# Performance work log

Hardware: AMD Instinct MI355X
Metric: run time of the kernel (lower is better)

## Reference

```python
import jax, jax.numpy as jnp
import numpy as np

N_NODES = 100000
N_EDGES = 1600000
G_DIM, H1_DIM, H2_DIM = 128, 64, 64
N_REL = 8          # 2 * n_speakers**2, n_speakers=2
N_BASES = 30


def setup_inputs() -> dict:
    key = jax.random.key(0)
    ks = jax.random.split(key, 12)
    sc = lambda *s: 1.0 / np.sqrt(s[0])
    return {
        "node_features": jax.random.normal(ks[0], (N_NODES, G_DIM), jnp.float32),
        "edge_index": jax.random.randint(ks[1], (2, N_EDGES), 0, N_NODES),
        "edge_norm": jax.random.uniform(ks[2], (N_EDGES,), jnp.float32),
        "edge_type": jax.random.randint(ks[3], (N_EDGES,), 0, N_REL),
        # RGCNConv params (basis decomposition)
        "basis": jax.random.normal(ks[4], (N_BASES, G_DIM, H1_DIM), jnp.float32) * sc(G_DIM),
        "comp": jax.random.normal(ks[5], (N_REL, N_BASES), jnp.float32) * sc(N_BASES),
        "root": jax.random.normal(ks[6], (G_DIM, H1_DIM), jnp.float32) * sc(G_DIM),
        "bias1": jnp.zeros((H1_DIM,), jnp.float32),
        # GraphConv params
        "w_rel": jax.random.normal(ks[7], (H1_DIM, H2_DIM), jnp.float32) * sc(H1_DIM),
        "b_rel": jnp.zeros((H2_DIM,), jnp.float32),
        "w_root": jax.random.normal(ks[8], (H1_DIM, H2_DIM), jnp.float32) * sc(H1_DIM),
    }


def reference(node_features, edge_index, edge_norm, edge_type,
              basis, comp, root, bias1, w_rel, b_rel, w_root):
    N = node_features.shape[0]
    src, dst = edge_index[0], edge_index[1]

    # ---- RGCNConv: per-relation mean aggregation, basis-decomposed weights ----
    W = jnp.einsum('rb,bio->rio', comp, basis)          # [R, g, h1]
    x_src = node_features[src]                           # [E, g] gather
    out1 = node_features @ root + bias1                  # root + bias
    for r in range(N_REL):                               # fixed small relation set
        m = (edge_type == r).astype(node_features.dtype)  # [E]
        s = jax.ops.segment_sum(x_src * m[:, None], dst, num_segments=N)  # [N, g]
        cnt = jax.ops.segment_sum(m, dst, num_segments=N)                 # [N]
        h = s / jnp.maximum(cnt, 1.0)[:, None]            # mean aggr (0 if no edges)
        out1 = out1 + h @ W[r]

    # ---- GraphConv: sum of x_j * edge_weight -> lin_rel, plus lin_root ----
    agg = jax.ops.segment_sum(out1[src] * edge_norm[:, None], dst, num_segments=N)
    out2 = agg @ w_rel + b_rel + out1 @ w_root
    return out2
```

## Files before the change

### kernel.cpp

```cpp
#include <hip/hip_runtime.h>
#include <hip/hip_bf16.h>

#define NN 100000
#define NE 1600000
#define GD 128
#define H1 64
#define H2 64
#define NREL 8
#define NBASES 30
#define NBTOT 576

#define NPB 256
#define NBUCK ((NN + NPB - 1) / NPB)
#define NWGA 128
#define ECHUNK ((NE + NWGA - 1) / NWGA)

typedef __attribute__((ext_vector_type(8))) short bf16x8;
typedef __attribute__((ext_vector_type(4))) float f32x4;

static __device__ __forceinline__ unsigned short f2bf(float x) {
    __hip_bfloat16 h = __float2bfloat16(x);
    return *reinterpret_cast<unsigned short*>(&h);
}
static __device__ __forceinline__ float bf2f(unsigned short u) {
    return __uint_as_float(((unsigned)u) << 16);
}
static __device__ __forceinline__ float bflo(unsigned u) {
    return __uint_as_float(u << 16);
}
static __device__ __forceinline__ float bfhi(unsigned u) {
    return __uint_as_float(u & 0xffff0000u);
}

__global__ void prep_kernel(const float* __restrict__ basis,
                            const float* __restrict__ comp,
                            const float* __restrict__ root,
                            const float* __restrict__ w_rel,
                            const float* __restrict__ w_root,
                            unsigned short* __restrict__ WcatT,
                            unsigned short* __restrict__ B2T)
{
    int idx = blockIdx.x * blockDim.x + threadIdx.x;
    const int totalW = NBTOT * GD;
    if (idx < totalW) {
        int c = idx / GD;
        int i = idx % GD;
        float v;
        if (c < NREL * H1) {
            int r = c >> 6, o = c & 63;
            float acc = 0.f;
            #pragma unroll 5
            for (int b = 0; b < NBASES; ++b)
                acc += comp[r * NBASES + b] * basis[(b * GD + i) * H1 + o];
            v = acc;
        } else {
            v = root[i * H1 + (c - NREL * H1)];
        }
        WcatT[idx] = f2bf(v);
    } else {
        int j = idx - totalW;
        if (j < H2 * GD) {
            int o = j / GD, i = j % GD;
            float v = (i < H1) ? w_rel[i * H2 + o] : w_root[(i - H1) * H2 + o];
            B2T[j] = f2bf(v);
        }
    }
}

__global__ __launch_bounds__(512)
void bucket_count(const int* __restrict__ ei, unsigned* __restrict__ bcnt)
{
    __shared__ unsigned l[NBUCK];
    int t = threadIdx.x;
    int c0 = blockIdx.x * ECHUNK;
    int c1 = c0 + ECHUNK; if (c1 > NE) c1 = NE;
    for (int i = t; i < NBUCK; i += 512) l[i] = 0;
    __syncthreads();
    for (int e = c0 + t; e < c1; e += 512)
        atomicAdd(&l[ei[NE + e] >> 8], 1u);
    __syncthreads();
    for (int i = t; i < NBUCK; i += 512)
        if (l[i]) atomicAdd(&bcnt[i], l[i]);
}

__global__ __launch_bounds__(512)
void bucket_scan(const unsigned* __restrict__ bcnt,
                 unsigned* __restrict__ boff,
                 unsigned* __restrict__ bcur,
                 unsigned* __restrict__ off)
{
    __shared__ unsigned s[512];
    int t = threadIdx.x;
    unsigned v = (t < NBUCK) ? bcnt[t] : 0u;
    s[t] = v;
    __syncthreads();
    for (int st = 1; st < 512; st <<= 1) {
        unsigned u = (t >= st) ? s[t - st] : 0u;
        __syncthreads();
        s[t] += u;
        __syncthreads();
    }
    if (t < NBUCK) { boff[t] = s[t] - v; bcur[t] = s[t] - v; }
    if (t == 511) { boff[NBUCK] = s[511]; off[NN] = s[511]; }
}

__global__ __launch_bounds__(512)
void partition_a(const int* __restrict__ ei, const int* __restrict__ et,
                 const float* __restrict__ enorm,
                 unsigned* __restrict__ bcur,
                 uint2* __restrict__ tmp)
{
    __shared__ unsigned lcnt[NBUCK], wbase[NBUCK], lcur[NBUCK];
    int t = threadIdx.x;
    int c0 = blockIdx.x * ECHUNK;
    int c1 = c0 + ECHUNK; if (c1 > NE) c1 = NE;
    for (int i = t; i < NBUCK; i += 512) { lcnt[i] = 0; lcur[i] = 0; }
    __syncthreads();
    for (int e = c0 + t; e < c1; e += 512) {
        int dst = ei[NE + e];
        atomicAdd(&lcnt[dst >> 8], 1u);
    }
    __syncthreads();
    for (int i = t; i < NBUCK; i += 512)
        wbase[i] = atomicAdd(&bcur[i], lcnt[i]);
    __syncthreads();
    for (int e = c0 + t; e < c1; e += 512) {
        int src = ei[e], dst = ei[NE + e], r = et[e];
        int b = dst >> 8;
        unsigned pos = wbase[b] + atomicAdd(&lcur[b], 1u);
        unsigned dl = (unsigned)(dst & (NPB - 1));
        tmp[pos] = make_uint2((dl << 24) | ((unsigned)src << 3) | (unsigned)r,
                              __float_as_uint(enorm[e]));
    }
}

__global__ __launch_bounds__(512)
void partition_b(const unsigned* __restrict__ boff,
                 const uint2* __restrict__ tmp,
                 uint2* __restrict__ csr,
                 unsigned* __restrict__ off,
                 unsigned* __restrict__ cnt)
{
    __shared__ unsigned lcnt[NPB * NREL];
    __shared__ unsigned sscan[256];
    __shared__ unsigned lcur[NPB];
    int b = blockIdx.x, t = threadIdx.x;
    int nlo = b * NPB;
    int nn = NN - nlo; if (nn > NPB) nn = NPB;
    for (int i = t; i < NPB * NREL; i += 512) lcnt[i] = 0;
    __syncthreads();
    unsigned bstart = boff[b], bend = boff[b + 1];
    for (unsigned j = bstart + t; j < bend; j += 512) {
        unsigned x = tmp[j].x;
        atomicAdd(&lcnt[((x >> 24) << 3) | (x & 7u)], 1u);
    }
    __syncthreads();
    unsigned tot = 0;
    if (t < 256) {
        if (t < nn) {
            #pragma unroll
            for (int r = 0; r < NREL; ++r) tot += lcnt[t * NREL + r];
        }
        sscan[t] = tot;
    }
    __syncthreads();
    for (int st = 1; st < 256; st <<= 1) {
        unsigned u = (t < 256 && t >= st) ? sscan[t - st] : 0u;
        __syncthreads();
        if (t < 256) sscan[t] += u;
        __syncthreads();
    }
    if (t < nn) {
        unsigned ex = bstart + sscan[t] - tot;
        off[nlo + t] = ex;
        lcur[t] = ex;
        *reinterpret_cast<uint4*>(&cnt[(size_t)(nlo + t) * NREL]) =
            *reinterpret_cast<uint4*>(&lcnt[t * NREL]);
        *reinterpret_cast<uint4*>(&cnt[(size_t)(nlo + t) * NREL + 4]) =
            *reinterpret_cast<uint4*>(&lcnt[t * NREL + 4]);
    }
    __syncthreads();
    for (unsigned j = bstart + t; j < bend; j += 512) {
        uint2 rec = tmp[j];
        unsigned dl = rec.x >> 24;
        unsigned p = atomicAdd(&lcur[dl], 1u);
        csr[p] = make_uint2(rec.x & 0x00FFFFFFu, rec.y);
    }
}

template<int MODE>
__global__ __launch_bounds__(256)
void mfma_gemm(const void* __restrict__ Avoid,
               const unsigned short* __restrict__ Bt,
               int M,
               const float* __restrict__ bias,
               unsigned short* __restrict__ y,
               unsigned short* __restrict__ root1b,
               float* __restrict__ out)
{
    constexpr int NT = (MODE == 0) ? 9 : 1;
    __shared__ unsigned short Alds[128 * 128];
    __shared__ unsigned short Blds[64 * 128];

    int tid = threadIdx.x;
    int m0 = blockIdx.x * 128;
    int w = tid >> 6, l = tid & 63;
    int lr = l & 15, lk = l >> 4;

    uint4 breg0, breg1, breg2, breg3;
    {
        int c0 = (0 * 256 + tid) >> 4, s0 = tid & 15;
        int c1 = (1 * 256 + tid) >> 4;
        int c2 = (2 * 256 + tid) >> 4;
        int c3 = (3 * 256 + tid) >> 4;
        breg0 = *reinterpret_cast<const uint4*>(&Bt[(size_t)c0 * GD + s0 * 8]);
        breg1 = *reinterpret_cast<const uint4*>(&Bt[(size_t)c1 * GD + s0 * 8]);
        breg2 = *reinterpret_cast<const uint4*>(&Bt[(size_t)c2 * GD + s0 * 8]);
        breg3 = *reinterpret_cast<const uint4*>(&Bt[(size_t)c3 * GD + s0 * 8]);
    }

    if (MODE == 0) {
        const float* A = (const float*)Avoid;
        #pragma unroll
        for (int p = 0; p < 16; ++p) {
            int f = p * 256 + tid;
            int r = f >> 5;
            int c4 = f & 31;
            float4 av = make_float4(0.f, 0.f, 0.f, 0.f);
            if (m0 + r < M)
                av = *reinterpret_cast<const float4*>(&A[(size_t)(m0 + r) * GD + c4 * 4]);
            ushort4 bv;
            bv.x = f2bf(av.x); bv.y = f2bf(av.y); bv.z = f2bf(av.z); bv.w = f2bf(av.w);
            int slot = (c4 >> 1) ^ (r & 7);
            int byte = r * 256 + (slot << 4) + ((c4 & 1) << 3);
            *reinterpret_cast<ushort4*>(reinterpret_cast<char*>(Alds) + byte) = bv;
        }
    } else {
        const unsigned short* A = (const unsigned short*)Avoid;
        #pragma unroll
        for (int p = 0; p < 8; ++p) {
            int f = p * 256 + tid;
            int r = f >> 4;
            int slot = f & 15;
            uint4 v = make_uint4(0u, 0u, 0u, 0u);
            if (m0 + r < M)
                v = *reinterpret_cast<const uint4*>(&A[(size_t)(m0 + r) * GD + slot * 8]);
            int byte = r * 256 + ((slot ^ (r & 7)) << 4);
            *reinterpret_cast<uint4*>(reinterpret_cast<char*>(Alds) + byte) = v;
        }
    }

    {
        int c = (0 * 256 + tid) >> 4, s = tid & 15;
        *reinterpret_cast<uint4*>(reinterpret_cast<char*>(Blds) + c * 256 + ((s ^ (c & 7)) << 4)) = breg0;
        c = (1 * 256 + tid) >> 4;
        *reinterpret_cast<uint4*>(reinterpret_cast<char*>(Blds) + c * 256 + ((s ^ (c & 7)) << 4)) = breg1;
        c = (2 * 256 + tid) >> 4;
        *reinterpret_cast<uint4*>(reinterpret_cast<char*>(Blds) + c * 256 + ((s ^ (c & 7)) << 4)) = breg2;
        c = (3 * 256 + tid) >> 4;
        *reinterpret_cast<uint4*>(reinterpret_cast<char*>(Blds) + c * 256 + ((s ^ (c & 7)) << 4)) = breg3;
    }
    asm volatile("s_waitcnt lgkmcnt(0)" ::: "memory");
    __builtin_amdgcn_sched_barrier(0);
    __builtin_amdgcn_s_barrier();
    __builtin_amdgcn_sched_barrier(0);

    #pragma unroll 1
    for (int nt = 0; nt < NT; ++nt) {
        if (nt + 1 < NT) {
            int c = (0 * 256 + tid) >> 4, s = tid & 15;
            breg0 = *reinterpret_cast<const uint4*>(&Bt[(size_t)((nt + 1) * 64 + c) * GD + s * 8]);
            c = (1 * 256 + tid) >> 4;
            breg1 = *reinterpret_cast<const uint4*>(&Bt[(size_t)((nt + 1) * 64 + c) * GD + s * 8]);
            c = (2 * 256 + tid) >> 4;
            breg2 = *reinterpret_cast<const uint4*>(&Bt[(size_t)((nt + 1) * 64 + c) * GD + s * 8]);
            c = (3 * 256 + tid) >> 4;
            breg3 = *reinterpret_cast<const uint4*>(&Bt[(size_t)((nt + 1) * 64 + c) * GD + s * 8]);
        }

        f32x4 acc[2][4];
        #pragma unroll
        for (int i = 0; i < 2; ++i)
            #pragma unroll
            for (int j = 0; j < 4; ++j)
                acc[i][j] = (f32x4){0.f, 0.f, 0.f, 0.f};

        #pragma unroll
        for (int ks = 0; ks < 4; ++ks) {
            int q = 4 * ks + lk;
            int sA = q ^ (lr & 7);
            bf16x8 a0 = *reinterpret_cast<const bf16x8*>(
                reinterpret_cast<char*>(Alds) + (w * 32 + 0 * 16 + lr) * 256 + (sA << 4));
            bf16x8 a1 = *reinterpret_cast<const bf16x8*>(
                reinterpret_cast<char*>(Alds) + (w * 32 + 1 * 16 + lr) * 256 + (sA << 4));
            #pragma unroll
            for (int cf = 0; cf < 4; ++cf) {
                bf16x8 b = *reinterpret_cast<const bf16x8*>(
                    reinterpret_cast<char*>(Blds) + (cf * 16 + lr) * 256 + (sA << 4));
                acc[0][cf] = __builtin_amdgcn_mfma_f32_16x16x32_bf16(b, a0, acc[0][cf], 0, 0, 0);
                acc[1][cf] = __builtin_amdgcn_mfma_f32_16x16x32_bf16(b, a1, acc[1][cf], 0, 0, 0);
            }
        }

        #pragma unroll
        for (int rf = 0; rf < 2; ++rf) {
            int row = m0 + w * 32 + rf * 16 + lr;
            if (row < M) {
                #pragma unroll
                for (int cf = 0; cf < 4; ++cf) {
                    int cb = cf * 16 + lk * 4;
                    f32x4 v = acc[rf][cf];
                    if (MODE == 0) {
                        if (nt < 8) {
                            ushort4 pv;
                            pv.x = f2bf(v[0]); pv.y = f2bf(v[1]);
                            pv.z = f2bf(v[2]); pv.w = f2bf(v[3]);
                            *reinterpret_cast<ushort4*>(&y[(size_t)row * 512 + nt * 64 + cb]) = pv;
                        } else {
                            float4 bb = *reinterpret_cast<const float4*>(&bias[cb]);
                            ushort4 pv;
                            pv.x = f2bf(v[0] + bb.x); pv.y = f2bf(v[1] + bb.y);
                            pv.z = f2bf(v[2] + bb.z); pv.w = f2bf(v[3] + bb.w);
                            *reinterpret_cast<ushort4*>(&root1b[(size_t)row * 64 + cb]) = pv;
                        }
                    } else {
                        float4 bb = *reinterpret_cast<const float4*>(&bias[cb]);
                        float4 ov;
                        ov.x = v[0] + bb.x; ov.y = v[1] + bb.y;
                        ov.z = v[2] + bb.z; ov.w = v[3] + bb.w;
                        *reinterpret_cast<float4*>(&out[(size_t)row * 64 + cb]) = ov;
                    }
                }
            }
        }

        if (nt + 1 < NT) {
            asm volatile("s_waitcnt lgkmcnt(0)" ::: "memory");
            __builtin_amdgcn_sched_barrier(0);
            __builtin_amdgcn_s_barrier();
            __builtin_amdgcn_sched_barrier(0);
            int c = (0 * 256 + tid) >> 4, s = tid & 15;
            *reinterpret_cast<uint4*>(reinterpret_cast<char*>(Blds) + c * 256 + ((s ^ (c & 7)) << 4)) = breg0;
            c = (1 * 256 + tid) >> 4;
            *reinterpret_cast<uint4*>(reinterpret_cast<char*>(Blds) + c * 256 + ((s ^ (c & 7)) << 4)) = breg1;
            c = (2 * 256 + tid) >> 4;
            *reinterpret_cast<uint4*>(reinterpret_cast<char*>(Blds) + c * 256 + ((s ^ (c & 7)) << 4)) = breg2;
            c = (3 * 256 + tid) >> 4;
            *reinterpret_cast<uint4*>(reinterpret_cast<char*>(Blds) + c * 256 + ((s ^ (c & 7)) << 4)) = breg3;
            asm volatile("s_waitcnt lgkmcnt(0)" ::: "memory");
            __builtin_amdgcn_sched_barrier(0);
            __builtin_amdgcn_s_barrier();
            __builtin_amdgcn_sched_barrier(0);
        }
    }
}

__global__ void rgcn_aggregate(const unsigned* __restrict__ off,
                               const uint2* __restrict__ csr,
                               const unsigned* __restrict__ cnt,
                               const unsigned short* __restrict__ y,
                               const unsigned short* __restrict__ root1b,
                               unsigned short* __restrict__ abuf)
{
    int gid = blockIdx.x * blockDim.x + threadIdx.x;
    int n = gid >> 6;
    int l = gid & 63;
    if (n >= NN) return;
    int g = l >> 4;
    int sl = l & 15;
    unsigned myc = (l < NREL) ? cnt[(size_t)n * NREL + l] : 1u;
    float myinv = 1.0f / (float)(myc > 0u ? myc : 1u);
    unsigned s = off[n], e = off[n + 1];
    float a0 = 0.f, a1 = 0.f, a2 = 0.f, a3 = 0.f;
    float b0 = 0.f, b1 = 0.f, b2 = 0.f, b3 = 0.f;
    unsigned i = s;
    for (; i + 8 <= e; i += 8) {
        uint2 rA = csr[i + g];
        uint2 rB = csr[i + 4 + g];
        uint2 vA = *reinterpret_cast<const uint2*>(&y[(size_t)rA.x * 64 + sl * 4]);
        uint2 vB = *reinterpret_cast<const uint2*>(&y[(size_t)rB.x * 64 + sl * 4]);
        float wA = __shfl(myinv, (int)(rA.x & 7));
        float wB = __shfl(myinv, (int)(rB.x & 7));
        a0 += wA * bflo(vA.x); a1 += wA * bfhi(vA.x);
        a2 += wA * bflo(vA.y); a3 += wA * bfhi(vA.y);
        b0 += wB * bflo(vB.x); b1 += wB * bfhi(vB.x);
        b2 += wB * bflo(vB.y); b3 += wB * bfhi(vB.y);
    }
    if (i + 4 <= e) {
        uint2 rA = csr[i + g];
        uint2 vA = *reinterpret_cast<const uint2*>(&y[(size_t)rA.x * 64 + sl * 4]);
        float wA = __shfl(myinv, (int)(rA.x & 7));
        a0 += wA * bflo(vA.x); a1 += wA * bfhi(vA.x);
        a2 += wA * bflo(vA.y); a3 += wA * bfhi(vA.y);
        i += 4;
    }
    if (i < e) {
        unsigned idx = i + (unsigned)g;
        bool valid = idx < e;
        uint2 r = csr[valid ? idx : i];
        uint2 v = *reinterpret_cast<const uint2*>(&y[(size_t)r.x * 64 + sl * 4]);
        float w = __shfl(myinv, (int)(r.x & 7));
        if (!valid) w = 0.f;
        b0 += w * bflo(v.x); b1 += w * bfhi(v.x);
        b2 += w * bflo(v.y); b3 += w * bfhi(v.y);
    }
    a0 += b0; a1 += b1; a2 += b2; a3 += b3;
    a0 += __shfl_xor(a0, 16); a0 += __shfl_xor(a0, 32);
    a1 += __shfl_xor(a1, 16); a1 += __shfl_xor(a1, 32);
    a2 += __shfl_xor(a2, 16); a2 += __shfl_xor(a2, 32);
    a3 += __shfl_xor(a3, 16); a3 += __shfl_xor(a3, 32);
    if (g == 0) {
        uint2 rb = *reinterpret_cast<const uint2*>(&root1b[(size_t)n * 64 + sl * 4]);
        ushort4 pv;
        pv.x = f2bf(bflo(rb.x) + a0);
        pv.y = f2bf(bfhi(rb.x) + a1);
        pv.z = f2bf(bflo(rb.y) + a2);
        pv.w = f2bf(bfhi(rb.y) + a3);
        *reinterpret_cast<ushort4*>(&abuf[(size_t)n * 128 + 64 + sl * 4]) = pv;
    }
}

__global__ void graph_aggregate(const unsigned* __restrict__ off,
                                const uint2* __restrict__ csr,
                                unsigned short* __restrict__ abuf)
{
    int gid = blockIdx.x * blockDim.x + threadIdx.x;
    int n = gid >> 6;
    int l = gid & 63;
    if (n >= NN) return;
    int g = l >> 4;
    int sl = l & 15;
    unsigned s = off[n], e = off[n + 1];
    float a0 = 0.f, a1 = 0.f, a2 = 0.f, a3 = 0.f;
    float b0 = 0.f, b1 = 0.f, b2 = 0.f, b3 = 0.f;
    unsigned i = s;
    for (; i + 8 <= e; i += 8) {
        uint2 rA = csr[i + g];
        uint2 rB = csr[i + 4 + g];
        uint2 vA = *reinterpret_cast<const uint2*>(&abuf[(size_t)(rA.x >> 3) * 128 + 64 + sl * 4]);
        uint2 vB = *reinterpret_cast<const uint2*>(&abuf[(size_t)(rB.x >> 3) * 128 + 64 + sl * 4]);
        float wA = __uint_as_float(rA.y);
        float wB = __uint_as_float(rB.y);
        a0 += wA * bflo(vA.x); a1 += wA * bfhi(vA.x);
        a2 += wA * bflo(vA.y); a3 += wA * bfhi(vA.y);
        b0 += wB * bflo(vB.x); b1 += wB * bfhi(vB.x);
        b2 += wB * bflo(vB.y); b3 += wB * bfhi(vB.y);
    }
    if (i + 4 <= e) {
        uint2 rA = csr[i + g];
        uint2 vA = *reinterpret_cast<const uint2*>(&abuf[(size_t)(rA.x >> 3) * 128 + 64 + sl * 4]);
        float wA = __uint_as_float(rA.y);
        a0 += wA * bflo(vA.x); a1 += wA * bfhi(vA.x);
        a2 += wA * bflo(vA.y); a3 += wA * bfhi(vA.y);
        i += 4;
    }
    if (i < e) {
        unsigned idx = i + (unsigned)g;
        bool valid = idx < e;
        uint2 r = csr[valid ? idx : i];
        uint2 v = *reinterpret_cast<const uint2*>(&abuf[(size_t)(r.x >> 3) * 128 + 64 + sl * 4]);
        float w = valid ? __uint_as_float(r.y) : 0.f;
        b0 += w * bflo(v.x); b1 += w * bfhi(v.x);
        b2 += w * bflo(v.y); b3 += w * bfhi(v.y);
    }
    a0 += b0; a1 += b1; a2 += b2; a3 += b3;
    a0 += __shfl_xor(a0, 16); a0 += __shfl_xor(a0, 32);
    a1 += __shfl_xor(a1, 16); a1 += __shfl_xor(a1, 32);
    a2 += __shfl_xor(a2, 16); a2 += __shfl_xor(a2, 32);
    a3 += __shfl_xor(a3, 16); a3 += __shfl_xor(a3, 32);
    if (g == 0) {
        ushort4 pv;
        pv.x = f2bf(a0); pv.y = f2bf(a1); pv.z = f2bf(a2); pv.w = f2bf(a3);
        *reinterpret_cast<ushort4*>(&abuf[(size_t)n * 128 + sl * 4]) = pv;
    }
}

extern "C" void kernel_launch(void* const* d_in, const int* in_sizes, int n_in,
                              void* d_out, int out_size, void* d_ws, size_t ws_size,
                              hipStream_t stream)
{
    const float* node_features = (const float*)d_in[0];
    const int*   edge_index    = (const int*)d_in[1];
    const float* edge_norm     = (const float*)d_in[2];
    const int*   edge_type     = (const int*)d_in[3];
    const float* basis         = (const float*)d_in[4];
    const float* comp          = (const float*)d_in[5];
    const float* root          = (const float*)d_in[6];
    const float* bias1         = (const float*)d_in[7];
    const float* w_rel         = (const float*)d_in[8];
    const float* b_rel         = (const float*)d_in[9];
    const float* w_root        = (const float*)d_in[10];
    float* out = (float*)d_out;

    char* ws = (char*)d_ws;
    size_t o = 0;
    auto alloc = [&](size_t bytes) -> void* {
        o = (o + 511) & ~(size_t)511;
        void* p = ws + o;
        o += bytes;
        return p;
    };
    unsigned short* WcatT = (unsigned short*)alloc((size_t)NBTOT * GD * 2);
    unsigned short* B2T   = (unsigned short*)alloc((size_t)H2 * GD * 2);
    unsigned* cnt      = (unsigned*)alloc((size_t)NN * NREL * 4);
    unsigned* off_     = (unsigned*)alloc((size_t)(NN + 1) * 4);
    unsigned* bcnt     = (unsigned*)alloc((size_t)NBUCK * 4);
    unsigned* boff     = (unsigned*)alloc((size_t)(NBUCK + 1) * 4);
    unsigned* bcur     = (unsigned*)alloc((size_t)NBUCK * 4);
    uint2*    csr      = (uint2*)alloc((size_t)NE * 8);
    unsigned short* y  = (unsigned short*)alloc((size_t)NN * 512 * 2);
    unsigned short* root1b = (unsigned short*)alloc((size_t)NN * 64 * 2);
    unsigned short* abuf = (unsigned short*)alloc((size_t)NN * 128 * 2);
    uint2*    tmp      = (uint2*)abuf;

    hipMemsetAsync(bcnt, 0, (size_t)NBUCK * 4, stream);

    prep_kernel<<<(NBTOT * GD + H2 * GD + 255) / 256, 256, 0, stream>>>(
        basis, comp, root, w_rel, w_root, WcatT, B2T);

    bucket_count<<<NWGA, 512, 0, stream>>>(edge_index, bcnt);
    bucket_scan<<<1, 512, 0, stream>>>(bcnt, boff, bcur, off_);
    partition_a<<<NWGA, 512, 0, stream>>>(edge_index, edge_type, edge_norm, bcur, tmp);
    partition_b<<<NBUCK, 512, 0, stream>>>(boff, tmp, csr, off_, cnt);

    int gblk = (NN + 127) / 128;
    mfma_gemm<0><<<gblk, 256, 0, stream>>>(node_features, WcatT, NN, bias1, y, root1b, nullptr);

    rgcn_aggregate<<<(NN * 64 + 255) / 256, 256, 0, stream>>>(off_, csr, cnt, y, root1b, abuf);

    graph_aggregate<<<(NN * 64 + 255) / 256, 256, 0, stream>>>(off_, csr, abuf);

    mfma_gemm<1><<<gblk, 256, 0, stream>>>(abuf, B2T, NN, b_rel, nullptr, nullptr, out);
}
```

Before: 248.5 us.

## Co-schedule edge partitioning with the node GEMM in fused multi-role kernels

Weight prep and bucket counting now run in one kernel, split by block index. The first GEMM (node features times concatenated relation and root weights) is split in half: one half runs alongside partition_a and the other alongside partition_b, using shared-memory carve-outs and block-index dispatch. The GEMM body is reworked for 512-thread blocks with 16 rows per wave, and the second GEMM becomes its own specialised kernel. The aim is to fill idle compute units during the atomic-heavy partition phases and to cut launch count, at the cost of a larger shared-memory footprint per block and possibly different occupancy for the partition work.

```diff
diff --git a/kernel.cpp b/kernel.cpp
--- a/kernel.cpp
+++ b/kernel.cpp
@@ -14,6 +14,9 @@
 #define NBUCK ((NN + NPB - 1) / NPB)
 #define NWGA 128
 #define ECHUNK ((NE + NWGA - 1) / NWGA)
+#define PREP_BLKS 160
+#define GBLK ((NN + 127) / 128)
+#define GHALF 391
 
 typedef __attribute__((ext_vector_type(8))) short bf16x8;
 typedef __attribute__((ext_vector_type(4))) float f32x4;
@@ -32,55 +35,57 @@
     return __uint_as_float(u & 0xffff0000u);
 }
 
-__global__ void prep_kernel(const float* __restrict__ basis,
-                            const float* __restrict__ comp,
-                            const float* __restrict__ root,
-                            const float* __restrict__ w_rel,
-                            const float* __restrict__ w_root,
-                            unsigned short* __restrict__ WcatT,
-                            unsigned short* __restrict__ B2T)
-{
-    int idx = blockIdx.x * blockDim.x + threadIdx.x;
-    const int totalW = NBTOT * GD;
-    if (idx < totalW) {
-        int c = idx / GD;
-        int i = idx % GD;
-        float v;
-        if (c < NREL * H1) {
-            int r = c >> 6, o = c & 63;
-            float acc = 0.f;
-            #pragma unroll 5
-            for (int b = 0; b < NBASES; ++b)
-                acc += comp[r * NBASES + b] * basis[(b * GD + i) * H1 + o];
-            v = acc;
-        } else {
-            v = root[i * H1 + (c - NREL * H1)];
-        }
-        WcatT[idx] = f2bf(v);
-    } else {
-        int j = idx - totalW;
-        if (j < H2 * GD) {
-            int o = j / GD, i = j % GD;
-            float v = (i < H1) ? w_rel[i * H2 + o] : w_root[(i - H1) * H2 + o];
-            B2T[j] = f2bf(v);
-        }
-    }
-}
-
 __global__ __launch_bounds__(512)
-void bucket_count(const int* __restrict__ ei, unsigned* __restrict__ bcnt)
+void fused_pre(const float* __restrict__ basis,
+               const float* __restrict__ comp,
+               const float* __restrict__ root,
+               const float* __restrict__ w_rel,
+               const float* __restrict__ w_root,
+               unsigned short* __restrict__ WcatT,
+               unsigned short* __restrict__ B2T,
+               const int* __restrict__ ei,
+               unsigned* __restrict__ bcnt)
 {
     __shared__ unsigned l[NBUCK];
     int t = threadIdx.x;
-    int c0 = blockIdx.x * ECHUNK;
-    int c1 = c0 + ECHUNK; if (c1 > NE) c1 = NE;
-    for (int i = t; i < NBUCK; i += 512) l[i] = 0;
-    __syncthreads();
-    for (int e = c0 + t; e < c1; e += 512)
-        atomicAdd(&l[ei[NE + e] >> 8], 1u);
-    __syncthreads();
-    for (int i = t; i < NBUCK; i += 512)
-        if (l[i]) atomicAdd(&bcnt[i], l[i]);
+    if (blockIdx.x < PREP_BLKS) {
+        int idx = blockIdx.x * 512 + t;
+        const int totalW = NBTOT * GD;
+        if (idx < totalW) {
+            int c = idx / GD;
+            int i = idx % GD;
+            float v;
+            if (c < NREL * H1) {
+                int r = c >> 6, o = c & 63;
+                float acc = 0.f;
+                #pragma unroll 5
+                for (int b = 0; b < NBASES; ++b)
+                    acc += comp[r * NBASES + b] * basis[(b * GD + i) * H1 + o];
+                v = acc;
+            } else {
+                v = root[i * H1 + (c - NREL * H1)];
+            }
+            WcatT[idx] = f2bf(v);
+        } else {
+            int j = idx - totalW;
+            if (j < H2 * GD) {
+                int o = j / GD, i = j % GD;
+                float v = (i < H1) ? w_rel[i * H2 + o] : w_root[(i - H1) * H2 + o];
+                B2T[j] = f2bf(v);
+            }
+        }
+    } else {
+        int chunk = blockIdx.x - PREP_BLKS;
+        int c0 = chunk * ECHUNK;
+        int c1 = c0 + ECHUNK; if (c1 > NE) c1 = NE;
+        for (int i = t; i < NBUCK; i += 512) l[i] = 0;
+        __syncthreads();
+        for (int e = c0 + t; e < c1; e += 512)
+            atomicAdd(&l[ei[NE + e] >> 8], 1u);
+        __syncthreads();
+        for (int i = t; i < NBUCK; i += 512)
+            if (l[i]) atomicAdd(&bcnt[i], l[i]);
+    }
 }
 
 __global__ __launch_bounds__(512)
@@ -104,15 +109,133 @@
     if (t == 511) { boff[NBUCK] = s[511]; off[NN] = s[511]; }
 }
 
-__global__ __launch_bounds__(512)
-void partition_a(const int* __restrict__ ei, const int* __restrict__ et,
-                 const float* __restrict__ enorm,
-                 unsigned* __restrict__ bcur,
-                 uint2* __restrict__ tmp)
-{
-    __shared__ unsigned lcnt[NBUCK], wbase[NBUCK], lcur[NBUCK];
+__device__ __forceinline__
+void gemm0_body(char* smem, int m0,
+                const float* __restrict__ A,
+                const unsigned short* __restrict__ Bt,
+                int M,
+                const float* __restrict__ bias,
+                unsigned short* __restrict__ y,
+                unsigned short* __restrict__ root1b)
+{
+    unsigned short* Alds = (unsigned short*)smem;
+    unsigned short* Blds = (unsigned short*)(smem + 32768);
+    int tid = threadIdx.x;
+    int w = tid >> 6, l = tid & 63;
+    int lr = l & 15, lk = l >> 4;
+
+    uint4 breg0, breg1;
+    {
+        int c0 = tid >> 4, s0 = tid & 15;
+        int c1 = 32 + (tid >> 4);
+        breg0 = *reinterpret_cast<const uint4*>(&Bt[(size_t)c0 * GD + s0 * 8]);
+        breg1 = *reinterpret_cast<const uint4*>(&Bt[(size_t)c1 * GD + s0 * 8]);
+    }
+
+    #pragma unroll
+    for (int p = 0; p < 8; ++p) {
+        int f = p * 512 + tid;
+        int r = f >> 5;
+        int c4 = f & 31;
+        float4 av = make_float4(0.f, 0.f, 0.f, 0.f);
+        if (m0 + r < M)
+            av = *reinterpret_cast<const float4*>(&A[(size_t)(m0 + r) * GD + c4 * 4]);
+        ushort4 bv;
+        bv.x = f2bf(av.x); bv.y = f2bf(av.y); bv.z = f2bf(av.z); bv.w = f2bf(av.w);
+        int slot = (c4 >> 1) ^ (r & 7);
+        int byte = r * 256 + (slot << 4) + ((c4 & 1) << 3);
+        *reinterpret_cast<ushort4*>(reinterpret_cast<char*>(Alds) + byte) = bv;
+    }
+
+    {
+        int c = tid >> 4, s = tid & 15;
+        *reinterpret_cast<uint4*>(reinterpret_cast<char*>(Blds) + c * 256 + ((s ^ (c & 7)) << 4)) = breg0;
+        c = 32 + (tid >> 4);
+        *reinterpret_cast<uint4*>(reinterpret_cast<char*>(Blds) + c * 256 + ((s ^ (c & 7)) << 4)) = breg1;
+    }
+    asm volatile("s_waitcnt lgkmcnt(0)" ::: "memory");
+    __builtin_amdgcn_sched_barrier(0);
+    __builtin_amdgcn_s_barrier();
+    __builtin_amdgcn_sched_barrier(0);
+
+    #pragma unroll 1
+    for (int nt = 0; nt < 9; ++nt) {
+        if (nt + 1 < 9) {
+            int c = tid >> 4, s = tid & 15;
+            breg0 = *reinterpret_cast<const uint4*>(&Bt[(size_t)((nt + 1) * 64 + c) * GD + s * 8]);
+            c = 32 + (tid >> 4);
+            breg1 = *reinterpret_cast<const uint4*>(&Bt[(size_t)((nt + 1) * 64 + c) * GD + s * 8]);
+        }
+
+        f32x4 acc[4];
+        #pragma unroll
+        for (int j = 0; j < 4; ++j)
+            acc[j] = (f32x4){0.f, 0.f, 0.f, 0.f};
+
+        #pragma unroll
+        for (int ks = 0; ks < 4; ++ks) {
+            int q = 4 * ks + lk;
+            int sA = q ^ (lr & 7);
+            bf16x8 a0 = *reinterpret_cast<const bf16x8*>(
+                reinterpret_cast<char*>(Alds) + (w * 16 + lr) * 256 + (sA << 4));
+            #pragma unroll
+            for (int cf = 0; cf < 4; ++cf) {
+                bf16x8 b = *reinterpret_cast<const bf16x8*>(
+                    reinterpret_cast<char*>(Blds) + (cf * 16 + lr) * 256 + (sA << 4));
+                acc[cf] = __builtin_amdgcn_mfma_f32_16x16x32_bf16(b, a0, acc[cf], 0, 0, 0);
+            }
+        }
+
+        int row = m0 + w * 16 + lr;
+        if (row < M) {
+            #pragma unroll
+            for (int cf = 0; cf < 4; ++cf) {
+                int cb = cf * 16 + lk * 4;
+                f32x4 v = acc[cf];
+                if (nt < 8) {
+                    ushort4 pv;
+                    pv.x = f2bf(v[0]); pv.y = f2bf(v[1]);
+                    pv.z = f2bf(v[2]); pv.w = f2bf(v[3]);
+                    *reinterpret_cast<ushort4*>(&y[(size_t)row * 512 + nt * 64 + cb]) = pv;
+                } else {
+                    float4 bb = *reinterpret_cast<const float4*>(&bias[cb]);
+                    ushort4 pv;
+                    pv.x = f2bf(v[0] + bb.x); pv.y = f2bf(v[1] + bb.y);
+                    pv.z = f2bf(v[2] + bb.z); pv.w = f2bf(v[3] + bb.w);
+                    *reinterpret_cast<ushort4*>(&root1b[(size_t)row * 64 + cb]) = pv;
+                }
+            }
+        }
+
+        if (nt + 1 < 9) {
+            asm volatile("s_waitcnt lgkmcnt(0)" ::: "memory");
+            __builtin_amdgcn_sched_barrier(0);
+            __builtin_amdgcn_s_barrier();
+            __builtin_amdgcn_sched_barrier(0);
+            int c = tid >> 4, s = tid & 15;
+            *reinterpret_cast<uint4*>(reinterpret_cast<char*>(Blds) + c * 256 + ((s ^ (c & 7)) << 4)) = breg0;
+            c = 32 + (tid >> 4);
+            *reinterpret_cast<uint4*>(reinterpret_cast<char*>(Blds) + c * 256 + ((s ^ (c & 7)) << 4)) = breg1;
+            asm volatile("s_waitcnt lgkmcnt(0)" ::: "memory");
+            __builtin_amdgcn_sched_barrier(0);
+            __builtin_amdgcn_s_barrier();
+            __builtin_amdgcn_sched_barrier(0);
+        }
+    }
+}
+
+__device__ __forceinline__
+void parta_body(char* smem, int chunk,
+                const int* __restrict__ ei, const int* __restrict__ et,
+                const float* __restrict__ enorm,
+                unsigned* __restrict__ bcur,
+                uint2* __restrict__ tmp)
+{
+    unsigned* lcnt  = (unsigned*)smem;
+    unsigned* wbase = (unsigned*)(smem + 1600);
+    unsigned* lcur  = (unsigned*)(smem + 3200);
     int t = threadIdx.x;
-    int c0 = blockIdx.x * ECHUNK;
+    int c0 = chunk * ECHUNK;
     int c1 = c0 + ECHUNK; if (c1 > NE) c1 = NE;
     for (int i = t; i < NBUCK; i += 512) { lcnt[i] = 0; lcur[i] = 0; }
     __syncthreads();
@@ -134,17 +257,18 @@
     }
 }
 
-__global__ __launch_bounds__(512)
-void partition_b(const unsigned* __restrict__ boff,
-                 const uint2* __restrict__ tmp,
-                 uint2* __restrict__ csr,
-                 unsigned* __restrict__ off,
-                 unsigned* __restrict__ cnt)
-{
-    __shared__ unsigned lcnt[NPB * NREL];
-    __shared__ unsigned sscan[256];
-    __shared__ unsigned lcur[NPB];
-    int b = blockIdx.x, t = threadIdx.x;
+__device__ __forceinline__
+void partb_body(char* smem, int b,
+                const unsigned* __restrict__ boff,
+                const uint2* __restrict__ tmp,
+                uint2* __restrict__ csr,
+                unsigned* __restrict__ off,
+                unsigned* __restrict__ cnt)
+{
+    unsigned* lcnt  = (unsigned*)smem;
+    unsigned* sscan = (unsigned*)(smem + 8192);
+    unsigned* lcur  = (unsigned*)(smem + 9216);
+    int t = threadIdx.x;
     int nlo = b * NPB;
     int nn = NN - nlo; if (nn > NPB) nn = NPB;
     for (int i = t; i < NPB * NREL; i += 512) lcnt[i] = 0;
@@ -188,17 +312,50 @@
     }
 }
 
-template<int MODE>
+__global__ __launch_bounds__(512)
+void fused_a(const int* __restrict__ ei, const int* __restrict__ et,
+             const float* __restrict__ enorm,
+             unsigned* __restrict__ bcur,
+             uint2* __restrict__ tmp,
+             const float* __restrict__ A,
+             const unsigned short* __restrict__ Bt,
+             const float* __restrict__ bias,
+             unsigned short* __restrict__ y,
+             unsigned short* __restrict__ root1b)
+{
+    __shared__ char smem[49152];
+    if (blockIdx.x < NWGA)
+        parta_body(smem, blockIdx.x, ei, et, enorm, bcur, tmp);
+    else
+        gemm0_body(smem, (int)(blockIdx.x - NWGA) * 128, A, Bt, NN, bias, y, root1b);
+}
+
+__global__ __launch_bounds__(512)
+void fused_b(const unsigned* __restrict__ boff,
+             const uint2* __restrict__ tmp,
+             uint2* __restrict__ csr,
+             unsigned* __restrict__ off,
+             unsigned* __restrict__ cnt,
+             const float* __restrict__ A,
+             const unsigned short* __restrict__ Bt,
+             const float* __restrict__ bias,
+             unsigned short* __restrict__ y,
+             unsigned short* __restrict__ root1b)
+{
+    __shared__ char smem[49152];
+    if (blockIdx.x < NBUCK)
+        partb_body(smem, blockIdx.x, boff, tmp, csr, off, cnt);
+    else
+        gemm0_body(smem, (int)blockIdx.x * 128, A, Bt, NN, bias, y, root1b);
+}
+
 __global__ __launch_bounds__(256)
-void mfma_gemm(const void* __restrict__ Avoid,
-               const unsigned short* __restrict__ Bt,
-               int M,
-               const float* __restrict__ bias,
-               unsigned short* __restrict__ y,
-               unsigned short* __restrict__ root1b,
-               float* __restrict__ out)
-{
-    constexpr int NT = (MODE == 0) ? 9 : 1;
+void mfma_gemm1(const unsigned short* __restrict__ A,
+                const unsigned short* __restrict__ Bt,
+                int M,
+                const float* __restrict__ bias,
+                float* __restrict__ out)
+{
     __shared__ unsigned short Alds[128 * 128];
     __shared__ unsigned short Blds[64 * 128];
 
@@ -219,35 +376,16 @@
         breg3 = *reinterpret_cast<const uint4*>(&Bt[(size_t)c3 * GD + s0 * 8]);
     }
 
-    if (MODE == 0) {
-        const float* A = (const float*)Avoid;
-        #pragma unroll
-        for (int p = 0; p < 16; ++p) {
-            int f = p * 256 + tid;
-            int r = f >> 5;
-            int c4 = f & 31;
-            float4 av = make_float4(0.f, 0.f, 0.f, 0.f);
-            if (m0 + r < M)
-                av = *reinterpret_cast<const float4*>(&A[(size_t)(m0 + r) * GD + c4 * 4]);
-            ushort4 bv;
-            bv.x = f2bf(av.x); bv.y = f2bf(av.y); bv.z = f2bf(av.z); bv.w = f2bf(av.w);
-            int slot = (c4 >> 1) ^ (r & 7);
-            int byte = r * 256 + (slot << 4) + ((c4 & 1) << 3);
-            *reinterpret_cast<ushort4*>(reinterpret_cast<char*>(Alds) + byte) = bv;
-        }
-    } else {
-        const unsigned short* A = (const unsigned short*)Avoid;
-        #pragma unroll
-        for (int p = 0; p < 8; ++p) {
-            int f = p * 256 + tid;
-            int r = f >> 4;
-            int slot = f & 15;
-            uint4 v = make_uint4(0u, 0u, 0u, 0u);
-            if (m0 + r < M)
-                v = *reinterpret_cast<const uint4*>(&A[(size_t)(m0 + r) * GD + slot * 8]);
-            int byte = r * 256 + ((slot ^ (r & 7)) << 4);
-            *reinterpret_cast<uint4*>(reinterpret_cast<char*>(Alds) + byte) = v;
-        }
+    #pragma unroll
+    for (int p = 0; p < 8; ++p) {
+        int f = p * 256 + tid;
+        int r = f >> 4;
+        int slot = f & 15;
+        uint4 v = make_uint4(0u, 0u, 0u, 0u);
+        if (m0 + r < M)
+            v = *reinterpret_cast<const uint4*>(&A[(size_t)(m0 + r) * GD + slot * 8]);
+        int byte = r * 256 + ((slot ^ (r & 7)) << 4);
+        *reinterpret_cast<uint4*>(reinterpret_cast<char*>(Alds) + byte) = v;
     }
 
     {
@@ -260,97 +398,46 @@
         c = (3 * 256 + tid) >> 4;
         *reinterpret_cast<uint4*>(reinterpret_cast<char*>(Blds) + c * 256 + ((s ^ (c & 7)) << 4)) = breg3;
     }
-    asm volatile("s_waitcnt lgkmcnt(0)" ::: "memory");
-    __builtin_amdgcn_sched_barrier(0);
-    __builtin_amdgcn_s_barrier();
-    __builtin_amdgcn_sched_barrier(0);
-
-    #pragma unroll 1
-    for (int nt = 0; nt < NT; ++nt) {
-        if (nt + 1 < NT) {
-            int c = (0 * 256 + tid) >> 4, s = tid & 15;
-            breg0 = *reinterpret_cast<const uint4*>(&Bt[(size_t)((nt + 1) * 64 + c) * GD + s * 8]);
-            c = (1 * 256 + tid) >> 4;
-            breg1 = *reinterpret_cast<const uint4*>(&Bt[(size_t)((nt + 1) * 64 + c) * GD + s * 8]);
-            c = (2 * 256 + tid) >> 4;
-            breg2 = *reinterpret_cast<const uint4*>(&Bt[(size_t)((nt + 1) * 64 + c) * GD + s * 8]);
-            c = (3 * 256 + tid) >> 4;
-            breg3 = *reinterpret_cast<const uint4*>(&Bt[(size_t)((nt + 1) * 64 + c) * GD + s * 8]);
-        }
-
-        f32x4 acc[2][4];
+    __syncthreads();
+
+    f32x4 acc[2][4];
+    #pragma unroll
+    for (int i = 0; i < 2; ++i)
         #pragma unroll
-        for (int i = 0; i < 2; ++i)
-            #pragma unroll
-            for (int j = 0; j < 4; ++j)
-                acc[i][j] = (f32x4){0.f, 0.f, 0.f, 0.f};
-
+        for (int j = 0; j < 4; ++j)
+            acc[i][j] = (f32x4){0.f, 0.f, 0.f, 0.f};
+
+    #pragma unroll
+    for (int ks = 0; ks < 4; ++ks) {
+        int q = 4 * ks + lk;
+        int sA = q ^ (lr & 7);
+        bf16x8 a0 = *reinterpret_cast<const bf16x8*>(
+            reinterpret_cast<char*>(Alds) + (w * 32 + 0 * 16 + lr) * 256 + (sA << 4));
+        bf16x8 a1 = *reinterpret_cast<const bf16x8*>(
+            reinterpret_cast<char*>(Alds) + (w * 32 + 1 * 16 + lr) * 256 + (sA << 4));
         #pragma unroll
-        for (int ks = 0; ks < 4; ++ks) {
-            int q = 4 * ks + lk;
-            int sA = q ^ (lr & 7);
-            bf16x8 a0 = *reinterpret_cast<const bf16x8*>(
-                reinterpret_cast<char*>(Alds) + (w * 32 + 0 * 16 + lr) * 256 + (sA << 4));
-            bf16x8 a1 = *reinterpret_cast<const bf16x8*>(
-                reinterpret_cast<char*>(Alds) + (w * 32 + 1 * 16 + lr) * 256 + (sA << 4));
+        for (int cf = 0; cf < 4; ++cf) {
+            bf16x8 b = *reinterpret_cast<const bf16x8*>(
+                reinterpret_cast<char*>(Blds) + (cf * 16 + lr) * 256 + (sA << 4));
+            acc[0][cf] = __builtin_amdgcn_mfma_f32_16x16x32_bf16(b, a0, acc[0][cf], 0, 0, 0);
+            acc[1][cf] = __builtin_amdgcn_mfma_f32_16x16x32_bf16(b, a1, acc[1][cf], 0, 0, 0);
+        }
+    }
+
+    #pragma unroll
+    for (int rf = 0; rf < 2; ++rf) {
+        int row = m0 + w * 32 + rf * 16 + lr;
+        if (row < M) {
             #pragma unroll
             for (int cf = 0; cf < 4; ++cf) {
-                bf16x8 b = *reinterpret_cast<const bf16x8*>(
-                    reinterpret_cast<char*>(Blds) + (cf * 16 + lr) * 256 + (sA << 4));
-                acc[0][cf] = __builtin_amdgcn_mfma_f32_16x16x32_bf16(b, a0, acc[0][cf], 0, 0, 0);
-                acc[1][cf] = __builtin_amdgcn_mfma_f32_16x16x32_bf16(b, a1, acc[1][cf], 0, 0, 0);
+                int cb = cf * 16 + lk * 4;
+                f32x4 v = acc[rf][cf];
+                float4 bb = *reinterpret_cast<const float4*>(&bias[cb]);
+                float4 ov;
+                ov.x = v[0] + bb.x; ov.y = v[1] + bb.y;
+                ov.z = v[2] + bb.z; ov.w = v[3] + bb.w;
+                *reinterpret_cast<float4*>(&out[(size_t)row * 64 + cb]) = ov;
             }
-        }
-
-        #pragma unroll
-        for (int rf = 0; rf < 2; ++rf) {
-            int row = m0 + w * 32 + rf * 16 + lr;
-            if (row < M) {
-                #pragma unroll
-                for (int cf = 0; cf < 4; ++cf) {
-                    int cb = cf * 16 + lk * 4;
-                    f32x4 v = acc[rf][cf];
-                    if (MODE == 0) {
-                        if (nt < 8) {
-                            ushort4 pv;
-                            pv.x = f2bf(v[0]); pv.y = f2bf(v[1]);
-                            pv.z = f2bf(v[2]); pv.w = f2bf(v[3]);
-                            *reinterpret_cast<ushort4*>(&y[(size_t)row * 512 + nt * 64 + cb]) = pv;
-                        } else {
-                            float4 bb = *reinterpret_cast<const float4*>(&bias[cb]);
-                            ushort4 pv;
-                            pv.x = f2bf(v[0] + bb.x); pv.y = f2bf(v[1] + bb.y);
-                            pv.z = f2bf(v[2] + bb.z); pv.w = f2bf(v[3] + bb.w);
-                            *reinterpret_cast<ushort4*>(&root1b[(size_t)row * 64 + cb]) = pv;
-                        }
-                    } else {
-                        float4 bb = *reinterpret_cast<const float4*>(&bias[cb]);
-                        float4 ov;
-                        ov.x = v[0] + bb.x; ov.y = v[1] + bb.y;
-                        ov.z = v[2] + bb.z; ov.w = v[3] + bb.w;
-                        *reinterpret_cast<float4*>(&out[(size_t)row * 64 + cb]) = ov;
-                    }
-                }
-            }
-        }
-
-        if (nt + 1 < NT) {
-            asm volatile("s_waitcnt lgkmcnt(0)" ::: "memory");
-            __builtin_amdgcn_sched_barrier(0);
-            __builtin_amdgcn_s_barrier();
-            __builtin_amdgcn_sched_barrier(0);
-            int c = (0 * 256 + tid) >> 4, s = tid & 15;
-            *reinterpret_cast<uint4*>(reinterpret_cast<char*>(Blds) + c * 256 + ((s ^ (c & 7)) << 4)) = breg0;
-            c = (1 * 256 + tid) >> 4;
-            *reinterpret_cast<uint4*>(reinterpret_cast<char*>(Blds) + c * 256 + ((s ^ (c & 7)) << 4)) = breg1;
-            c = (2 * 256 + tid) >> 4;
-            *reinterpret_cast<uint4*>(reinterpret_cast<char*>(Blds) + c * 256 + ((s ^ (c & 7)) << 4)) = breg2;
-            c = (3 * 256 + tid) >> 4;
-            *reinterpret_cast<uint4*>(reinterpret_cast<char*>(Blds) + c * 256 + ((s ^ (c & 7)) << 4)) = breg3;
-            asm volatile("s_waitcnt lgkmcnt(0)" ::: "memory");
-            __builtin_amdgcn_sched_barrier(0);
-            __builtin_amdgcn_s_barrier();
-            __builtin_amdgcn_sched_barrier(0);
         }
     }
 }
@@ -513,22 +600,24 @@
     unsigned short* abuf = (unsigned short*)alloc((size_t)NN * 128 * 2);
     uint2*    tmp      = (uint2*)abuf;
 
-    hipMemsetAsync(bcnt, 0, (size_t)NBUCK * 4, stream);
-
-    prep_kernel<<<(NBTOT * GD + H2 * GD + 255) / 256, 256, 0, stream>>>(
-        basis, comp, root, w_rel, w_root, WcatT, B2T);
-
-    bucket_count<<<NWGA, 512, 0, stream>>>(edge_index, bcnt);
+    (void)hipMemsetAsync(bcnt, 0, (size_t)NBUCK * 4, stream);
+
+    fused_pre<<<PREP_BLKS + NWGA, 512, 0, stream>>>(
+        basis, comp, root, w_rel, w_root, WcatT, B2T, edge_index, bcnt);
+
     bucket_scan<<<1, 512, 0, stream>>>(bcnt, boff, bcur, off_);
-    partition_a<<<NWGA, 512, 0, stream>>>(edge_index, edge_type, edge_norm, bcur, tmp);
-    partition_b<<<NBUCK, 512, 0, stream>>>(boff, tmp, csr, off_, cnt);
-
-    int gblk = (NN + 127) / 128;
-    mfma_gemm<0><<<gblk, 256, 0, stream>>>(node_features, WcatT, NN, bias1, y, root1b, nullptr);
+
+    fused_a<<<NWGA + GHALF, 512, 0, stream>>>(
+        edge_index, edge_type, edge_norm, bcur, tmp,
+        node_features, WcatT, bias1, y, root1b);
+
+    fused_b<<<GBLK, 512, 0, stream>>>(
+        boff, tmp, csr, off_, cnt,
+        node_features, WcatT, bias1, y, root1b);
 
     rgcn_aggregate<<<(NN * 64 + 255) / 256, 256, 0, stream>>>(off_, csr, cnt, y, root1b, abuf);
 
     graph_aggregate<<<(NN * 64 + 255) / 256, 256, 0, stream>>>(off_, csr, abuf);
 
-    mfma_gemm<1><<<gblk, 256, 0, stream>>>(abuf, B2T, NN, b_rel, nullptr, nullptr, out);
-}
+    mfma_gemm1<<<GBLK, 256, 0, stream>>>(abuf, B2T, NN, b_rel, out);
+}
```

After: 254.7 us. 1.02x slower.
